# Optimization experiments

Measured on AMD Instinct MI355X. Metric: run time of the kernel, lower is better.

Reference implementation:

```python
import jax, jax.numpy as jnp
import numpy as np

C = 128

def setup_inputs() -> dict:
    key = jax.random.key(0)
    ks = jax.random.split(key, 7)
    x = jax.random.normal(ks[0], (4, 64, 64, C), dtype=jnp.float32)
    s = 1.0 / np.sqrt(C)
    Wq = jax.random.normal(ks[1], (C, C), dtype=jnp.float32) * s
    bq = jnp.zeros((C,), dtype=jnp.float32)
    Wk = jax.random.normal(ks[2], (C, C), dtype=jnp.float32) * s
    bk = jnp.zeros((C,), dtype=jnp.float32)
    Wv = jax.random.normal(ks[3], (C, C), dtype=jnp.float32) * s
    bv = jnp.zeros((C,), dtype=jnp.float32)
    return {"x": x, "Wq": Wq, "bq": bq, "Wk": Wk, "bk": bk, "Wv": Wv, "bv": bv}

def reference(x, Wq, bq, Wk, bk, Wv, bv):
    B, H, W, Cc = x.shape
    N = H * W
    xt = x.reshape(B, N, Cc)  # 1x1 conv == per-token linear
    q = xt @ Wq + bq
    k = xt @ Wk + bk
    v = xt @ Wv + bv
    scale = jnp.sqrt(jnp.asarray(Cc, dtype=x.dtype))
    attn = jnp.einsum('bnc,bmc->bnm', q, k) / scale  # [B, N, N]
    attn = jax.nn.softmax(attn, axis=-1)
    out = jnp.einsum('bnm,bmc->bnc', attn, v)
    return x + out.reshape(B, H, W, Cc)
```

## Files before the change

### kernel.cpp

```cpp
#include <hip/hip_runtime.h>

constexpr int C       = 128;
constexpr int N       = 4096;
constexpr int BATCH   = 4;
constexpr int TOTROWS = BATCH * N;
constexpr float SCALE = 0.08838834764831845f;
constexpr float LOG2E = 1.44269504088896340736f;

constexpr int BK = 64;

typedef __attribute__((ext_vector_type(8))) short        bf16x8;
typedef __attribute__((ext_vector_type(4))) float        f32x4;
typedef __attribute__((ext_vector_type(2))) unsigned int u32x2;

__device__ inline unsigned short f2bf(float f) {
    unsigned int u = __float_as_uint(f);
    return (unsigned short)((u + 0x7FFFu + ((u >> 16) & 1u)) >> 16);
}
__device__ inline unsigned int cvtpk(float a, float b) {
    unsigned int r;
    asm("v_cvt_pk_bf16_f32 %0, %1, %2" : "=v"(r) : "v"(a), "v"(b));
    return r;
}
__device__ inline float bf2f(unsigned int u) {
    return __uint_as_float(u << 16);
}
__device__ inline float fexp2(float x) {
#if __has_builtin(__builtin_amdgcn_exp2f)
    return __builtin_amdgcn_exp2f(x);
#else
    float r; asm("v_exp_f32 %0, %1\n\ts_nop 0" : "=v"(r) : "v"(x)); return r;
#endif
}
__device__ inline void dma16(const void* g, void* l) {
    __builtin_amdgcn_global_load_lds(
        (const __attribute__((address_space(1))) void*)g,
        (__attribute__((address_space(3))) void*)l, 16, 0, 0);
}

__global__ __launch_bounds__(256)
void qkv_kernel(const float* __restrict__ x,
                const float* __restrict__ Wq, const float* __restrict__ bq,
                const float* __restrict__ Wk, const float* __restrict__ bk,
                const float* __restrict__ Wv, const float* __restrict__ bv,
                unsigned short* __restrict__ qo,
                unsigned short* __restrict__ ko,
                unsigned short* __restrict__ vt)
{
    constexpr int TS = 136;
    __shared__ __align__(16) unsigned short wl[128 * TS];

    const int tid  = threadIdx.x;
    const int wv   = tid >> 6;
    const int lane = tid & 63;
    const int lo   = lane & 15;
    const int quad = lane >> 4;
    const int mat  = blockIdx.y;
    const long rowbase = (long)blockIdx.x * 64 + wv * 16;

    const float* W    = (mat == 0) ? Wq : (mat == 1) ? Wk : Wv;
    const float* bias = (mat == 0) ? bq : (mat == 1) ? bk : bv;
    const float  s    = (mat == 0) ? SCALE * LOG2E : 1.0f;

    bf16x8 xf[4];
    {
        const float4* xr = reinterpret_cast<const float4*>(&x[(rowbase + lo) * C]);
        #pragma unroll
        for (int ks = 0; ks < 4; ++ks) {
            float4 a  = xr[ks * 8 + quad * 2];
            float4 b2 = xr[ks * 8 + quad * 2 + 1];
            union { bf16x8 v; unsigned int u[4]; } cv;
            cv.u[0] = cvtpk(a.x, a.y);
            cv.u[1] = cvtpk(a.z, a.w);
            cv.u[2] = cvtpk(b2.x, b2.y);
            cv.u[3] = cvtpk(b2.z, b2.w);
            xf[ks] = cv.v;
        }
    }

    #pragma unroll
    for (int g = 0; g < 16; ++g) {
        int idx = g * 256 + tid;
        int i = idx >> 5, c4 = (idx & 31) * 4;
        float4 a = *reinterpret_cast<const float4*>(&W[i * 128 + c4]);
        wl[(c4 + 0) * TS + i] = f2bf(a.x * s);
        wl[(c4 + 1) * TS + i] = f2bf(a.y * s);
        wl[(c4 + 2) * TS + i] = f2bf(a.z * s);
        wl[(c4 + 3) * TS + i] = f2bf(a.w * s);
    }
    __syncthreads();

    if (mat < 2) {
        f32x4 acc[8] = {};
        #pragma unroll
        for (int ks = 0; ks < 4; ++ks)
            #pragma unroll
            for (int mt = 0; mt < 8; ++mt) {
                bf16x8 wf = *reinterpret_cast<const bf16x8*>(
                    &wl[(mt * 16 + lo) * TS + ks * 32 + quad * 8]);
                acc[mt] = __builtin_amdgcn_mfma_f32_16x16x32_bf16(
                    wf, xf[ks], acc[mt], 0, 0, 0);
            }
        unsigned short* out = (mat == 0) ? qo : ko;
        long row = rowbase + lo;
        #pragma unroll
        for (int mt = 0; mt < 8; ++mt) {
            float4 bb = *reinterpret_cast<const float4*>(&bias[mt * 16 + quad * 4]);
            u32x2 w;
            w[0] = cvtpk(acc[mt][0] + bb.x * s, acc[mt][1] + bb.y * s);
            w[1] = cvtpk(acc[mt][2] + bb.z * s, acc[mt][3] + bb.w * s);
            *reinterpret_cast<u32x2*>(&out[row * C + mt * 16 + quad * 4]) = w;
        }
    } else {
        f32x4 acc[8] = {};
        #pragma unroll
        for (int ks = 0; ks < 4; ++ks)
            #pragma unroll
            for (int ct = 0; ct < 8; ++ct) {
                bf16x8 wf = *reinterpret_cast<const bf16x8*>(
                    &wl[(ct * 16 + lo) * TS + ks * 32 + quad * 8]);
                acc[ct] = __builtin_amdgcn_mfma_f32_16x16x32_bf16(
                    xf[ks], wf, acc[ct], 0, 0, 0);
            }
        const int b = (int)(rowbase >> 12);
        const int nbase = (int)(rowbase & (N - 1));
        const int n0   = nbase + quad * 4;
        const int nblk = n0 >> 6;
        #pragma unroll
        for (int ct = 0; ct < 8; ++ct) {
            int chan = ct * 16 + lo;
            float bb = bias[chan];
            u32x2 w;
            w[0] = cvtpk(acc[ct][0] + bb, acc[ct][1] + bb);
            w[1] = cvtpk(acc[ct][2] + bb, acc[ct][3] + bb);
            *reinterpret_cast<u32x2*>(
                &vt[(((size_t)b * 64 + nblk) * 128 + chan) * 64 + (n0 & 63)]) = w;
        }
    }
}

__global__ __launch_bounds__(256, 2)
void attn_kernel(const unsigned short* __restrict__ q,
                 const unsigned short* __restrict__ k,
                 const unsigned short* __restrict__ vt,
                 unsigned short* __restrict__ opart,
                 float* __restrict__ lpart)
{
    __shared__ __align__(16) unsigned short smA[17472];
    __shared__ __align__(16) unsigned short smB[16384];
    __shared__ __align__(16) unsigned short smP[4096];

    const int tid  = threadIdx.x;
    const int wv   = tid >> 6;
    const int lane = tid & 63;
    const int lo   = lane & 15;
    const int quad = lane >> 4;

    const int nspl = (int)(gridDim.x >> 7);
    const int id   = blockIdx.x;
    int b, sl, qt;
    if (nspl == 4) {
        b  = (id >> 1) & 3;
        sl = (id & 1) | (((id >> 3) & 1) << 1);
        qt = id >> 4;
    } else {
        b  = (id >> 1) & 3;
        sl = id & 1;
        qt = id >> 3;
    }
    const int NIT  = (N / nspl) / BK;
    const int koff = sl * (N / nspl);

    const int    rowb  = b * N + qt * 128;
    const size_t qrow0 = (size_t)rowb + wv * 32;
    const unsigned short* kb  = k  + ((size_t)b * N + koff) * C;
    const unsigned short* vtb = vt + ((size_t)b * 64 + (koff >> 6)) * (size_t)(128 * 64);
    const char* kb8 = (const char*)kb;
    const char* vb8 = (const char*)vtb;

    unsigned short* PW = smP + wv * 1024;

    bf16x8 qf[2][4];
    #pragma unroll
    for (int nt = 0; nt < 2; ++nt)
        #pragma unroll
        for (int ks = 0; ks < 4; ++ks)
            qf[nt][ks] = *reinterpret_cast<const bf16x8*>(
                &q[(qrow0 + nt * 16 + lo) * C + ks * 32 + quad * 8]);

    int offK[4], offV[4];
    #pragma unroll
    for (int c = 0; c < 4; ++c) {
        int G  = (wv * 4 + c) * 64 + lane;
        int kr = G >> 4;
        offK[c] = kr * 256 + (((G & 15) ^ (kr & 7)) << 4);
        int vr = G >> 3;
        offV[c] = vr * 128 + (((G & 7) ^ (vr & 7)) << 4);
    }

    auto stage = [&](int kt, unsigned short* dstKV) {
        const char* kt8 = kb8 + kt * 16384;
        const char* vt8 = vb8 + kt * 16384;
        #pragma unroll
        for (int c = 0; c < 4; ++c)
            dma16(kt8 + offK[c], dstKV + (wv * 4 + c) * 512);
        #pragma unroll
        for (int c = 0; c < 4; ++c)
            dma16(vt8 + offV[c], dstKV + 8192 + (wv * 4 + c) * 512);
    };

    float l_i[2] = { 0.f, 0.f };
    f32x4 ot[2][8] = {};

    auto body = [&](const unsigned short* base) {
        const unsigned short* kc = base;
        const unsigned short* vc = base + 8192;

        f32x4 st[4][2] = {};
        #pragma unroll
        for (int ks = 0; ks < 4; ++ks)
            #pragma unroll
            for (int mt = 0; mt < 4; ++mt) {
                const bf16x8 kf = *reinterpret_cast<const bf16x8*>(
                    &kc[(mt * 16 + lo) * 128 + (((ks * 4 + quad) ^ (lo & 7)) << 3)]);
                #pragma unroll
                for (int nt = 0; nt < 2; ++nt)
                    st[mt][nt] = __builtin_amdgcn_mfma_f32_16x16x32_bf16(
                        kf, qf[nt][ks], st[mt][nt], 0, 0, 0);
            }

        #pragma unroll
        for (int h = 0; h < 2; ++h) {
            #pragma unroll
            for (int nt = 0; nt < 2; ++nt) {
                const int prow = nt * 16 + lo;
                float ps = 0.f;
                #pragma unroll
                for (int m = 0; m < 2; ++m) {
                    f32x4 s = st[2 * h + m][nt];
                    float p0 = fexp2(s[0]);
                    float p1 = fexp2(s[1]);
                    float p2 = fexp2(s[2]);
                    float p3 = fexp2(s[3]);
                    ps += (p0 + p1) + (p2 + p3);
                    u32x2 w;
                    w[0] = cvtpk(p0, p1);
                    w[1] = cvtpk(p2, p3);
                    *reinterpret_cast<u32x2*>(
                        &PW[prow * 32 + (((2 * m + (quad >> 1)) ^ (prow & 3)) << 3)
                            + (quad & 1) * 4]) = w;
                }
                l_i[nt] += ps;
            }
            bf16x8 pf[2];
            #pragma unroll
            for (int nt = 0; nt < 2; ++nt) {
                const int prow = nt * 16 + lo;
                pf[nt] = *reinterpret_cast<const bf16x8*>(
                    &PW[prow * 32 + ((quad ^ (prow & 3)) << 3)]);
            }
            #pragma unroll
            for (int ct = 0; ct < 8; ++ct) {
                const bf16x8 vf = *reinterpret_cast<const bf16x8*>(
                    &vc[(ct * 16 + lo) * 64 + (((h * 4 + quad) ^ (lo & 7)) << 3)]);
                #pragma unroll
                for (int nt = 0; nt < 2; ++nt)
                    ot[nt][ct] = __builtin_amdgcn_mfma_f32_16x16x32_bf16(
                        vf, pf[nt], ot[nt][ct], 0, 0, 0);
            }
        }
    };

    stage(0, smA);
    __syncthreads();
    for (int kt = 0; kt < NIT; kt += 2) {
        stage(kt + 1, smB);
        body(smA);
        __syncthreads();
        if (kt + 2 < NIT) stage(kt + 2, smA);
        body(smB);
        __syncthreads();
    }

    #pragma unroll
    for (int nt = 0; nt < 2; ++nt) {
        l_i[nt] += __shfl_xor(l_i[nt], 16);
        l_i[nt] += __shfl_xor(l_i[nt], 32);
    }
    if (quad == 0) {
        #pragma unroll
        for (int nt = 0; nt < 2; ++nt)
            lpart[(size_t)sl * TOTROWS + qrow0 + nt * 16 + lo] = l_i[nt];
    }

    constexpr int OSTR = 136;
    unsigned short* obl = smA;
    #pragma unroll
    for (int nt = 0; nt < 2; ++nt) {
        const int row = wv * 32 + nt * 16 + lo;
        #pragma unroll
        for (int ct = 0; ct < 8; ++ct) {
            u32x2 w;
            w[0] = cvtpk(ot[nt][ct][0], ot[nt][ct][1]);
            w[1] = cvtpk(ot[nt][ct][2], ot[nt][ct][3]);
            *reinterpret_cast<u32x2*>(&obl[row * OSTR + ct * 16 + quad * 4]) = w;
        }
    }
    __syncthreads();
    {
        unsigned short* obg = opart + (size_t)sl * TOTROWS * C;
        const int row  = tid >> 1;
        const int half = tid & 1;
        const unsigned short* src = &obl[row * OSTR + half * 64];
        unsigned short*       dst = &obg[((size_t)rowb + row) * C + half * 64];
        #pragma unroll
        for (int i = 0; i < 8; ++i)
            *reinterpret_cast<uint4*>(&dst[i * 8]) =
                *reinterpret_cast<const uint4*>(&src[i * 8]);
    }
}

__global__ __launch_bounds__(256)
void combine_kernel(const float* __restrict__ x,
                    const unsigned short* __restrict__ opart,
                    const float* __restrict__ lpart,
                    float* __restrict__ out, int nspl)
{
    int gid = blockIdx.x * 256 + threadIdx.x;
    int row = gid >> 5;
    int c4  = (gid & 31) * 4;

    float denom = 0.f;
    for (int j = 0; j < nspl; ++j) denom += lpart[(size_t)j * TOTROWS + row];
    float inv = 1.0f / denom;

    size_t idx = (size_t)row * C + c4;
    float a0 = 0.f, a1 = 0.f, a2 = 0.f, a3 = 0.f;
    for (int j = 0; j < nspl; ++j) {
        u32x2 o = *reinterpret_cast<const u32x2*>(
            &opart[(size_t)j * TOTROWS * C + idx]);
        a0 += bf2f(o[0] & 0xffff);
        a1 += bf2f(o[0] >> 16);
        a2 += bf2f(o[1] & 0xffff);
        a3 += bf2f(o[1] >> 16);
    }
    float4 xv = *reinterpret_cast<const float4*>(&x[idx]);
    float4 o;
    o.x = xv.x + a0 * inv;
    o.y = xv.y + a1 * inv;
    o.z = xv.z + a2 * inv;
    o.w = xv.w + a3 * inv;
    *reinterpret_cast<float4*>(&out[idx]) = o;
}

extern "C" void kernel_launch(void* const* d_in, const int* in_sizes, int n_in,
                              void* d_out, int out_size, void* d_ws, size_t ws_size,
                              hipStream_t stream)
{
    const float* x  = (const float*)d_in[0];
    const float* Wq = (const float*)d_in[1];
    const float* bq = (const float*)d_in[2];
    const float* Wk = (const float*)d_in[3];
    const float* bk = (const float*)d_in[4];
    const float* Wv = (const float*)d_in[5];
    const float* bv = (const float*)d_in[6];
    float* out = (float*)d_out;

    const int nspl = (ws_size >= ((size_t)31 << 20)) ? 4 : 2;

    const size_t SPLIT_BYTES = (size_t)TOTROWS * C * 2;
    char* ws = (char*)d_ws;
    unsigned short* opart = (unsigned short*)ws;
    char* base = ws + (size_t)nspl * SPLIT_BYTES;
    unsigned short* q  = (unsigned short*)(base);
    unsigned short* k  = (unsigned short*)(base + SPLIT_BYTES);
    unsigned short* vt = (unsigned short*)(base + 2 * SPLIT_BYTES);
    float*          lp = (float*)(base + 3 * SPLIT_BYTES);

    qkv_kernel<<<dim3(TOTROWS / 64, 3), 256, 0, stream>>>(
        x, Wq, bq, Wk, bk, Wv, bv, q, k, vt);
    attn_kernel<<<nspl * 128, 256, 0, stream>>>(q, k, vt, opart, lp);
    combine_kernel<<<TOTROWS * 32 / 256, 256, 0, stream>>>(x, opart, lp, out, nspl);
}
```

Baseline: 133.1 us.

## Pre-convert QKV weights once and double-buffer them into LDS via DMA

A small new kernel converts, scales, transposes and swizzles the three weight matrices to bf16 once per call, into a workspace region. The QKV kernel now covers all three matrices in one block, loading x only once. It streams each prepared weight matrix into double-buffered LDS with global_load_lds DMA, replacing the per-block scalar fp32 conversion and transposed scattered LDS stores. This trades an extra launch and more LDS per block for less redundant weight conversion and x reads, and it assumes the workspace has room past the lpart buffer.

```diff
diff --git a/kernel.cpp b/kernel.cpp
--- a/kernel.cpp
+++ b/kernel.cpp
@@ -39,28 +39,48 @@
 }
 
 __global__ __launch_bounds__(256)
-void qkv_kernel(const float* __restrict__ x,
-                const float* __restrict__ Wq, const float* __restrict__ bq,
-                const float* __restrict__ Wk, const float* __restrict__ bk,
-                const float* __restrict__ Wv, const float* __restrict__ bv,
+void wprep_kernel(const float* __restrict__ Wq, const float* __restrict__ Wk,
+                  const float* __restrict__ Wv, unsigned short* __restrict__ wt)
+{
+    const int mat = blockIdx.x;
+    const float* W = (mat == 0) ? Wq : (mat == 1) ? Wk : Wv;
+    const float  s = (mat == 0) ? SCALE * LOG2E : 1.0f;
+    unsigned short* dst = wt + mat * 16384;
+
+    const int t  = threadIdx.x;
+    const int i0 = t >> 1;
+    const int ch = (t & 1) * 64;
+    const float4* src = reinterpret_cast<const float4*>(&W[i0 * 128 + ch]);
+    const int gsw = ((i0 >> 3) << 3) + (i0 & 7);
+    #pragma unroll
+    for (int jv = 0; jv < 16; ++jv) {
+        float4 a = src[jv];
+        float v[4] = { a.x * s, a.y * s, a.z * s, a.w * s };
+        #pragma unroll
+        for (int e = 0; e < 4; ++e) {
+            int o = ch + jv * 4 + e;
+            dst[o * 128 + ((((i0 >> 3) ^ ((o >> 2) & 7))) << 3) + (i0 & 7)] =
+                f2bf(v[e]);
+        }
+    }
+    (void)gsw;
+}
+
+__global__ __launch_bounds__(256, 2)
+void qkv_kernel(const float* __restrict__ x, const unsigned short* __restrict__ wt,
+                const float* __restrict__ bq, const float* __restrict__ bk,
+                const float* __restrict__ bv,
                 unsigned short* __restrict__ qo,
                 unsigned short* __restrict__ ko,
                 unsigned short* __restrict__ vt)
 {
-    constexpr int TS = 136;
-    __shared__ __align__(16) unsigned short wl[128 * TS];
+    __shared__ __align__(16) unsigned short wl[2][16384];
 
     const int tid  = threadIdx.x;
-    const int wv   = tid >> 6;
     const int lane = tid & 63;
     const int lo   = lane & 15;
     const int quad = lane >> 4;
-    const int mat  = blockIdx.y;
-    const long rowbase = (long)blockIdx.x * 64 + wv * 16;
-
-    const float* W    = (mat == 0) ? Wq : (mat == 1) ? Wk : Wv;
-    const float* bias = (mat == 0) ? bq : (mat == 1) ? bk : bv;
-    const float  s    = (mat == 0) ? SCALE * LOG2E : 1.0f;
+    const long rowbase = (long)blockIdx.x * 64 + (tid >> 6) * 16;
 
     bf16x8 xf[4];
     {
@@ -78,64 +98,73 @@
         }
     }
 
-    #pragma unroll
-    for (int g = 0; g < 16; ++g) {
-        int idx = g * 256 + tid;
-        int i = idx >> 5, c4 = (idx & 31) * 4;
-        float4 a = *reinterpret_cast<const float4*>(&W[i * 128 + c4]);
-        wl[(c4 + 0) * TS + i] = f2bf(a.x * s);
-        wl[(c4 + 1) * TS + i] = f2bf(a.y * s);
-        wl[(c4 + 2) * TS + i] = f2bf(a.z * s);
-        wl[(c4 + 3) * TS + i] = f2bf(a.w * s);
-    }
+    auto stageW = [&](int mat, int bufi) {
+        const char* src = (const char*)(wt + mat * 16384);
+        #pragma unroll
+        for (int c = 0; c < 8; ++c)
+            dma16(src + (c * 256 + tid) * 16, &wl[bufi][(c * 256 + tid) * 8]);
+    };
+
+    stageW(0, 0);
     __syncthreads();
 
-    if (mat < 2) {
-        f32x4 acc[8] = {};
-        #pragma unroll
-        for (int ks = 0; ks < 4; ++ks)
+    #pragma unroll
+    for (int mat = 0; mat < 3; ++mat) {
+        if (mat < 2) stageW(mat + 1, (mat + 1) & 1);
+        const unsigned short* wb = wl[mat & 1];
+
+        if (mat < 2) {
+            f32x4 acc[8] = {};
+            #pragma unroll
+            for (int ks = 0; ks < 4; ++ks)
+                #pragma unroll
+                for (int mt = 0; mt < 8; ++mt) {
+                    const int rr = mt * 16 + lo;
+                    bf16x8 wf = *reinterpret_cast<const bf16x8*>(
+                        &wb[rr * 128 + (((ks * 4 + quad) ^ ((rr >> 2) & 7)) << 3)]);
+                    acc[mt] = __builtin_amdgcn_mfma_f32_16x16x32_bf16(
+                        wf, xf[ks], acc[mt], 0, 0, 0);
+                }
+            const float* bias = (mat == 0) ? bq : bk;
+            const float  s    = (mat == 0) ? SCALE * LOG2E : 1.0f;
+            unsigned short* out = (mat == 0) ? qo : ko;
+            long row = rowbase + lo;
             #pragma unroll
             for (int mt = 0; mt < 8; ++mt) {
-                bf16x8 wf = *reinterpret_cast<const bf16x8*>(
-                    &wl[(mt * 16 + lo) * TS + ks * 32 + quad * 8]);
-                acc[mt] = __builtin_amdgcn_mfma_f32_16x16x32_bf16(
-                    wf, xf[ks], acc[mt], 0, 0, 0);
-            }
-        unsigned short* out = (mat == 0) ? qo : ko;
-        long row = rowbase + lo;
-        #pragma unroll
-        for (int mt = 0; mt < 8; ++mt) {
-            float4 bb = *reinterpret_cast<const float4*>(&bias[mt * 16 + quad * 4]);
-            u32x2 w;
-            w[0] = cvtpk(acc[mt][0] + bb.x * s, acc[mt][1] + bb.y * s);
-            w[1] = cvtpk(acc[mt][2] + bb.z * s, acc[mt][3] + bb.w * s);
-            *reinterpret_cast<u32x2*>(&out[row * C + mt * 16 + quad * 4]) = w;
+                float4 bb = *reinterpret_cast<const float4*>(&bias[mt * 16 + quad * 4]);
+                u32x2 w;
+                w[0] = cvtpk(acc[mt][0] + bb.x * s, acc[mt][1] + bb.y * s);
+                w[1] = cvtpk(acc[mt][2] + bb.z * s, acc[mt][3] + bb.w * s);
+                *reinterpret_cast<u32x2*>(&out[row * C + mt * 16 + quad * 4]) = w;
+            }
+        } else {
+            f32x4 acc[8] = {};
+            #pragma unroll
+            for (int ks = 0; ks < 4; ++ks)
+                #pragma unroll
+                for (int ct = 0; ct < 8; ++ct) {
+                    const int rr = ct * 16 + lo;
+                    bf16x8 wf = *reinterpret_cast<const bf16x8*>(
+                        &wb[rr * 128 + (((ks * 4 + quad) ^ ((rr >> 2) & 7)) << 3)]);
+                    acc[ct] = __builtin_amdgcn_mfma_f32_16x16x32_bf16(
+                        xf[ks], wf, acc[ct], 0, 0, 0);
+                }
+            const int b = (int)(rowbase >> 12);
+            const int nbase = (int)(rowbase & (N - 1));
+            const int n0   = nbase + quad * 4;
+            const int nblk = n0 >> 6;
+            #pragma unroll
+            for (int ct = 0; ct < 8; ++ct) {
+                int chan = ct * 16 + lo;
+                float bb = bv[chan];
+                u32x2 w;
+                w[0] = cvtpk(acc[ct][0] + bb, acc[ct][1] + bb);
+                w[1] = cvtpk(acc[ct][2] + bb, acc[ct][3] + bb);
+                *reinterpret_cast<u32x2*>(
+                    &vt[(((size_t)b * 64 + nblk) * 128 + chan) * 64 + (n0 & 63)]) = w;
+            }
         }
-    } else {
-        f32x4 acc[8] = {};
-        #pragma unroll
-        for (int ks = 0; ks < 4; ++ks)
-            #pragma unroll
-            for (int ct = 0; ct < 8; ++ct) {
-                bf16x8 wf = *reinterpret_cast<const bf16x8*>(
-                    &wl[(ct * 16 + lo) * TS + ks * 32 + quad * 8]);
-                acc[ct] = __builtin_amdgcn_mfma_f32_16x16x32_bf16(
-                    xf[ks], wf, acc[ct], 0, 0, 0);
-            }
-        const int b = (int)(rowbase >> 12);
-        const int nbase = (int)(rowbase & (N - 1));
-        const int n0   = nbase + quad * 4;
-        const int nblk = n0 >> 6;
-        #pragma unroll
-        for (int ct = 0; ct < 8; ++ct) {
-            int chan = ct * 16 + lo;
-            float bb = bias[chan];
-            u32x2 w;
-            w[0] = cvtpk(acc[ct][0] + bb, acc[ct][1] + bb);
-            w[1] = cvtpk(acc[ct][2] + bb, acc[ct][3] + bb);
-            *reinterpret_cast<u32x2*>(
-                &vt[(((size_t)b * 64 + nblk) * 128 + chan) * 64 + (n0 & 63)]) = w;
-        }
+        __syncthreads();
     }
 }
 
@@ -173,10 +202,8 @@
 
     const int    rowb  = b * N + qt * 128;
     const size_t qrow0 = (size_t)rowb + wv * 32;
-    const unsigned short* kb  = k  + ((size_t)b * N + koff) * C;
-    const unsigned short* vtb = vt + ((size_t)b * 64 + (koff >> 6)) * (size_t)(128 * 64);
-    const char* kb8 = (const char*)kb;
-    const char* vb8 = (const char*)vtb;
+    const char* kb8 = (const char*)(k  + ((size_t)b * N + koff) * C);
+    const char* vb8 = (const char*)(vt + ((size_t)b * 64 + (koff >> 6)) * (size_t)(128 * 64));
 
     unsigned short* PW = smP + wv * 1024;
 
@@ -376,9 +403,11 @@
     unsigned short* k  = (unsigned short*)(base + SPLIT_BYTES);
     unsigned short* vt = (unsigned short*)(base + 2 * SPLIT_BYTES);
     float*          lp = (float*)(base + 3 * SPLIT_BYTES);
-
-    qkv_kernel<<<dim3(TOTROWS / 64, 3), 256, 0, stream>>>(
-        x, Wq, bq, Wk, bk, Wv, bv, q, k, vt);
+    unsigned short* wt = (unsigned short*)(base + 3 * SPLIT_BYTES
+                                           + (size_t)nspl * TOTROWS * 4);
+
+    wprep_kernel<<<3, 256, 0, stream>>>(Wq, Wk, Wv, wt);
+    qkv_kernel<<<TOTROWS / 64, 256, 0, stream>>>(x, wt, bq, bk, bv, q, k, vt);
     attn_kernel<<<nspl * 128, 256, 0, stream>>>(q, k, vt, opart, lp);
     combine_kernel<<<TOTROWS * 32 / 256, 256, 0, stream>>>(x, opart, lp, out, nspl);
 }
```

Result: no change. 132.9 us (-0.2%).
